# Optimization experiments

Measured on AMD Instinct MI355X. Metric: run time of the kernel, lower is better.

Reference implementation:

```python
import jax, jax.numpy as jnp
import numpy as np

B, C, FH, FW = 8, 256, 64, 64   # sketch/ref feature maps (B, C, F_H, F_W)
N = 131072                       # ~B*FH*FW*4 triplets, as the nested loops produce
MARGIN = 12.0


def setup_inputs() -> dict:
    key = jax.random.key(0)
    k1, k2, k3, k4, k5, k6 = jax.random.split(key, 6)
    sketch_query_vectors = jax.random.normal(k1, (B, C, FH, FW), jnp.float32)
    ref_key_vectors = jax.random.normal(k2, (B, C, FH, FW), jnp.float32)
    # Precomputed triplet indices. In the original these come from GridProcessing
    # (CPU grid math on G + random.choices negatives); they are constants w.r.t.
    # the float inputs, so we sample them once here.
    batch_idx = jax.random.randint(k3, (N,), 0, B, jnp.int32)
    anchor_yx = jax.random.randint(k4, (N, 2), 0, FH, jnp.int32)
    pos_yx = jax.random.randint(k5, (N, 2), 0, FH, jnp.int32)
    neg_yx = jax.random.randint(k6, (N, 2), 0, FH, jnp.int32)
    return {
        "sketch_query_vectors": sketch_query_vectors,
        "ref_key_vectors": ref_key_vectors,
        "batch_idx": batch_idx,
        "anchor_yx": anchor_yx,
        "pos_yx": pos_yx,
        "neg_yx": neg_yx,
    }


def reference(sketch_query_vectors, ref_key_vectors, batch_idx, anchor_yx, pos_yx, neg_yx):
    # Gather per-triplet feature vectors: [N, C]
    a = sketch_query_vectors[batch_idx, :, anchor_yx[:, 0], anchor_yx[:, 1]]
    p = ref_key_vectors[batch_idx, :, pos_yx[:, 0], pos_yx[:, 1]]
    n = ref_key_vectors[batch_idx, :, neg_yx[:, 0], neg_yx[:, 1]]
    dp = jnp.sum((a - p) ** 2, axis=-1)  # squared-euclidean, as calc_euclidean
    dn = jnp.sum((a - n) ** 2, axis=-1)
    losses = jax.nn.relu(dp - dn + MARGIN)  # per-triplet hinge (1-elem mean in orig)
    return jnp.sum(losses) / (1e-6 + N)
```

## Files before the change

kernel.cpp:

```cpp
#include <hip/hip_runtime.h>

#define NB 8
#define NC 256
#define FH 64
#define FW 64
#define NS (FH * FW)
#define NSAMP 131072
#define MARGIN_F 12.0f
#define GATHER_BLOCKS (NSAMP / 32)

typedef float vfloat2 __attribute__((ext_vector_type(2)));

__device__ __forceinline__ unsigned pack4_fp8(float f0, float f1, float f2, float f3)
{
    int r = __builtin_amdgcn_cvt_pk_fp8_f32(f0, f1, 0, false);
    r     = __builtin_amdgcn_cvt_pk_fp8_f32(f2, f3, r, true);
    return (unsigned)r;
}

__global__ __launch_bounds__(256) void transpose_to_bsc_fp8(
    const float* __restrict__ in0, const float* __restrict__ in1,
    unsigned char* __restrict__ out0, unsigned char* __restrict__ out1)
{
    __shared__ float tile[64][65];

    const int which = blockIdx.z >> 3;
    const int b     = blockIdx.z & 7;
    const float* __restrict__ in  = which ? in1 : in0;
    unsigned char* __restrict__ out = which ? out1 : out0;

    const int s0 = blockIdx.x * 64;
    const int c0 = blockIdx.y * 64;
    const int t  = threadIdx.x;

    const float* __restrict__ inb  = in  + (size_t)b * NC * NS;
    unsigned char* __restrict__ outb = out + (size_t)b * NS * NC;

    const int g   = t >> 4;
    const int sl4 = (t & 15) << 2;
#pragma unroll
    for (int pass = 0; pass < 4; ++pass) {
        const int cl = pass * 16 + g;
        const float4 v = *(const float4*)&inb[(size_t)(c0 + cl) * NS + (s0 + sl4)];
        tile[sl4 + 0][cl] = v.x;
        tile[sl4 + 1][cl] = v.y;
        tile[sl4 + 2][cl] = v.z;
        tile[sl4 + 3][cl] = v.w;
    }
    __syncthreads();

    const int cl4 = (t & 15) << 2;
#pragma unroll
    for (int pass = 0; pass < 4; ++pass) {
        const int sl = pass * 16 + (t >> 4);
        const unsigned w = pack4_fp8(tile[sl][cl4 + 0], tile[sl][cl4 + 1],
                                     tile[sl][cl4 + 2], tile[sl][cl4 + 3]);
        *(unsigned*)&outb[(size_t)(s0 + sl) * NC + (c0 + cl4)] = w;
    }
}

__device__ __forceinline__ void acc_u32(unsigned a, unsigned p, unsigned n, float& d)
{
    const vfloat2 a0 = __builtin_amdgcn_cvt_pk_f32_fp8(a, false);
    const vfloat2 a1 = __builtin_amdgcn_cvt_pk_f32_fp8(a, true);
    const vfloat2 p0 = __builtin_amdgcn_cvt_pk_f32_fp8(p, false);
    const vfloat2 p1 = __builtin_amdgcn_cvt_pk_f32_fp8(p, true);
    const vfloat2 n0 = __builtin_amdgcn_cvt_pk_f32_fp8(n, false);
    const vfloat2 n1 = __builtin_amdgcn_cvt_pk_f32_fp8(n, true);
    float t;
    t = a0.x - p0.x; d += t * t;  t = a0.x - n0.x; d -= t * t;
    t = a0.y - p0.y; d += t * t;  t = a0.y - n0.y; d -= t * t;
    t = a1.x - p1.x; d += t * t;  t = a1.x - n1.x; d -= t * t;
    t = a1.y - p1.y; d += t * t;  t = a1.y - n1.y; d -= t * t;
}

__device__ __forceinline__ void acc_quad(uint4 a, uint4 p, uint4 n, float& d)
{
    acc_u32(a.x, p.x, n.x, d);
    acc_u32(a.y, p.y, n.y, d);
    acc_u32(a.z, p.z, n.z, d);
    acc_u32(a.w, p.w, n.w, d);
}

__global__ __launch_bounds__(256) void triplet_gather_fp8(
    const uint4* __restrict__ tq,
    const uint4* __restrict__ tk,
    const int*  __restrict__ batch_idx,
    const int2* __restrict__ anchor_yx,
    const int2* __restrict__ pos_yx,
    const int2* __restrict__ neg_yx,
    float* __restrict__ partials)
{
    const int t    = threadIdx.x;
    const int ol   = t & 7;
    const int oct  = t >> 3;
    const int samp = blockIdx.x * 32 + oct;

    const int  b  = batch_idx[samp];
    const int2 ay = anchor_yx[samp];
    const int2 py = pos_yx[samp];
    const int2 ny = neg_yx[samp];

    const size_t ab = ((size_t)(b * NS) + ay.x * FW + ay.y) * 16;
    const size_t pb = ((size_t)(b * NS) + py.x * FW + py.y) * 16;
    const size_t nb = ((size_t)(b * NS) + ny.x * FW + ny.y) * 16;

    const uint4 A0 = tq[ab + ol];
    const uint4 A1 = tq[ab + 8 + ol];
    const uint4 P0 = tk[pb + ol];
    const uint4 P1 = tk[pb + 8 + ol];
    const uint4 N0 = tk[nb + ol];
    const uint4 N1 = tk[nb + 8 + ol];

    float d = 0.0f;
    acc_quad(A0, P0, N0, d);
    acc_quad(A1, P1, N1, d);

#pragma unroll
    for (int m = 1; m < 8; m <<= 1) d += __shfl_xor(d, m, 64);

    __shared__ float part[32];
    if (ol == 0) part[oct] = fmaxf(d + MARGIN_F, 0.0f);
    __syncthreads();
    if (t == 0) {
        float s = 0.0f;
#pragma unroll
        for (int i = 0; i < 32; ++i) s += part[i];
        partials[blockIdx.x] = s;
    }
}

__global__ __launch_bounds__(256) void final_reduce(
    const float* __restrict__ partials, float* __restrict__ out)
{
    float s = 0.0f;
    for (int i = threadIdx.x; i < GATHER_BLOCKS; i += 256) s += partials[i];
#pragma unroll
    for (int m = 1; m < 64; m <<= 1) s += __shfl_xor(s, m, 64);
    __shared__ float ws4[4];
    if ((threadIdx.x & 63) == 0) ws4[threadIdx.x >> 6] = s;
    __syncthreads();
    if (threadIdx.x == 0) {
        const float invN = 1.0f / (1e-6f + (float)NSAMP);
        out[0] = (ws4[0] + ws4[1] + ws4[2] + ws4[3]) * invN;
    }
}

__global__ __launch_bounds__(256) void triplet_direct(
    const float* __restrict__ q, const float* __restrict__ k,
    const int*  __restrict__ batch_idx,
    const int2* __restrict__ anchor_yx,
    const int2* __restrict__ pos_yx,
    const int2* __restrict__ neg_yx,
    float* __restrict__ out)
{
    const int lane   = threadIdx.x & 63;
    const int wid    = threadIdx.x >> 6;
    const int gwave  = blockIdx.x * 4 + wid;
    const int nwaves = gridDim.x * 4;

    float wsum = 0.0f;
    for (int i = gwave; i < NSAMP; i += nwaves) {
        const int  b  = batch_idx[i];
        const int2 ay = anchor_yx[i];
        const int2 py = pos_yx[i];
        const int2 ny = neg_yx[i];

        const size_t base = (size_t)b * NC * NS;
        const int sa = ay.x * FW + ay.y;
        const int sp = py.x * FW + py.y;
        const int sn = ny.x * FW + ny.y;

        float d = 0.0f;
#pragma unroll
        for (int kk = 0; kk < 4; ++kk) {
            const int c = lane + 64 * kk;
            const float av = q[base + (size_t)c * NS + sa];
            const float pv = k[base + (size_t)c * NS + sp];
            const float nv = k[base + (size_t)c * NS + sn];
            float t;
            t = av - pv; d += t * t;
            t = av - nv; d -= t * t;
        }
#pragma unroll
        for (int m = 1; m < 64; m <<= 1) d += __shfl_xor(d, m, 64);
        if (lane == 0) wsum += fmaxf(d + MARGIN_F, 0.0f);
    }

    __shared__ float bsum[4];
    if (lane == 0) bsum[wid] = wsum;
    __syncthreads();
    if (threadIdx.x == 0) {
        const float invN = 1.0f / (1e-6f + (float)NSAMP);
        atomicAdd(out, (bsum[0] + bsum[1] + bsum[2] + bsum[3]) * invN);
    }
}

extern "C" void kernel_launch(void* const* d_in, const int* in_sizes, int n_in,
                              void* d_out, int out_size, void* d_ws, size_t ws_size,
                              hipStream_t stream)
{
    const float* sketch = (const float*)d_in[0];
    const float* refk   = (const float*)d_in[1];
    const int*   bidx   = (const int*)d_in[2];
    const int2*  ayx    = (const int2*)d_in[3];
    const int2*  pyx    = (const int2*)d_in[4];
    const int2*  nyx    = (const int2*)d_in[5];
    float*       out    = (float*)d_out;

    const size_t tensor_elems = (size_t)NB * NC * NS;
    const size_t need = 2 * tensor_elems * sizeof(unsigned char)
                      + GATHER_BLOCKS * sizeof(float);

    if (ws_size >= need) {
        unsigned char* tq = (unsigned char*)d_ws;
        unsigned char* tk = tq + tensor_elems;
        float* partials = (float*)(tk + tensor_elems);

        dim3 tgrid(NS / 64, NC / 64, 16);
        transpose_to_bsc_fp8<<<tgrid, 256, 0, stream>>>(sketch, refk, tq, tk);

        triplet_gather_fp8<<<GATHER_BLOCKS, 256, 0, stream>>>(
            (const uint4*)tq, (const uint4*)tk, bidx, ayx, pyx, nyx, partials);

        final_reduce<<<1, 256, 0, stream>>>(partials, out);
    } else {
        (void)hipMemsetAsync(out, 0, sizeof(float), stream);
        triplet_direct<<<4096, 256, 0, stream>>>(
            sketch, refk, bidx, ayx, pyx, nyx, out);
    }
}
```

Measured before the change: 123.3 us.

## Bucket triplets by batch so each XCD gathers from one batch slice

Adds a bucketing pass that sorts triplet index records by batch into per-batch arrays using shared and global atomic cursors. The gather kernel then maps blockIdx&7 to a batch, so under round-robin XCD dispatch each XCD only touches one batch's fp8 feature slice, which should improve L2 locality. The final reduce kernel is replaced by an atomicAdd per block. The cost is an extra kernel, two memsets, record writes and reads, and a data-dependent strided loop. The mapping assumes blocks are dispatched to XCDs round-robin.

Measured after the change: 170.1 us. 1.38x slower.

```diff
diff --git a/kernel.cpp b/kernel.cpp
--- a/kernel.cpp
+++ b/kernel.cpp
@@ -7,7 +7,12 @@
 #define NS (FH * FW)
 #define NSAMP 131072
 #define MARGIN_F 12.0f
-#define GATHER_BLOCKS (NSAMP / 32)
+
+#define BUCKET_CAP NSAMP
+#define GATHER_BLOCKS 4096
+#define GROUPS_PER_XCD (GATHER_BLOCKS / 8)
+#define OCTETS_PER_BLOCK 32
+#define BUCKET_STRIDE (GROUPS_PER_XCD * OCTETS_PER_BLOCK)
 
 typedef float vfloat2 __attribute__((ext_vector_type(2)));
 
@@ -57,6 +62,35 @@
                                      tile[sl][cl4 + 2], tile[sl][cl4 + 3]);
         *(unsigned*)&outb[(size_t)(s0 + sl) * NC + (c0 + cl4)] = w;
     }
+}
+
+__global__ __launch_bounds__(256) void bucket_samples(
+    const int*  __restrict__ batch_idx,
+    const int2* __restrict__ anchor_yx,
+    const int2* __restrict__ pos_yx,
+    const int2* __restrict__ neg_yx,
+    uint4* __restrict__ recs,
+    unsigned* __restrict__ cursors)
+{
+    const int i = blockIdx.x * 256 + threadIdx.x;
+    const int  b  = batch_idx[i];
+    const int2 ay = anchor_yx[i];
+    const int2 py = pos_yx[i];
+    const int2 ny = neg_yx[i];
+
+    const unsigned aoff = (unsigned)(b * NS + ay.x * FW + ay.y);
+    const unsigned poff = (unsigned)(b * NS + py.x * FW + py.y);
+    const unsigned noff = (unsigned)(b * NS + ny.x * FW + ny.y);
+
+    __shared__ unsigned hist[8], base[8];
+    if (threadIdx.x < 8) hist[threadIdx.x] = 0;
+    __syncthreads();
+    const unsigned rank = atomicAdd(&hist[b], 1u);
+    __syncthreads();
+    if (threadIdx.x < 8)
+        base[threadIdx.x] = atomicAdd(&cursors[threadIdx.x], hist[threadIdx.x]);
+    __syncthreads();
+    recs[(size_t)b * BUCKET_CAP + base[b] + rank] = make_uint4(aoff, poff, noff, 0u);
 }
 
 __device__ __forceinline__ void acc_u32(unsigned a, unsigned p, unsigned n, float& d)
@@ -82,67 +116,52 @@
     acc_u32(a.w, p.w, n.w, d);
 }
 
-__global__ __launch_bounds__(256) void triplet_gather_fp8(
+__global__ __launch_bounds__(256) void triplet_gather_xcd(
     const uint4* __restrict__ tq,
     const uint4* __restrict__ tk,
-    const int*  __restrict__ batch_idx,
-    const int2* __restrict__ anchor_yx,
-    const int2* __restrict__ pos_yx,
-    const int2* __restrict__ neg_yx,
-    float* __restrict__ partials)
-{
-    const int t    = threadIdx.x;
-    const int ol   = t & 7;
-    const int oct  = t >> 3;
-    const int samp = blockIdx.x * 32 + oct;
-
-    const int  b  = batch_idx[samp];
-    const int2 ay = anchor_yx[samp];
-    const int2 py = pos_yx[samp];
-    const int2 ny = neg_yx[samp];
-
-    const size_t ab = ((size_t)(b * NS) + ay.x * FW + ay.y) * 16;
-    const size_t pb = ((size_t)(b * NS) + py.x * FW + py.y) * 16;
-    const size_t nb = ((size_t)(b * NS) + ny.x * FW + ny.y) * 16;
-
-    const uint4 A0 = tq[ab + ol];
-    const uint4 A1 = tq[ab + 8 + ol];
-    const uint4 P0 = tk[pb + ol];
-    const uint4 P1 = tk[pb + 8 + ol];
-    const uint4 N0 = tk[nb + ol];
-    const uint4 N1 = tk[nb + 8 + ol];
-
-    float d = 0.0f;
-    acc_quad(A0, P0, N0, d);
-    acc_quad(A1, P1, N1, d);
-
-#pragma unroll
-    for (int m = 1; m < 8; m <<= 1) d += __shfl_xor(d, m, 64);
-
-    __shared__ float part[32];
-    if (ol == 0) part[oct] = fmaxf(d + MARGIN_F, 0.0f);
+    const uint4* __restrict__ recs,
+    const unsigned* __restrict__ cursors,
+    float* __restrict__ out)
+{
+    const int t   = threadIdx.x;
+    const int ol  = t & 7;
+    const int oct = t >> 3;
+    const int x   = blockIdx.x & 7;
+    const int g   = blockIdx.x >> 3;
+
+    const unsigned cnt = cursors[x];
+    const uint4* __restrict__ brecs = recs + (size_t)x * BUCKET_CAP;
+
+    float acc = 0.0f;
+    for (unsigned j = (unsigned)(g * OCTETS_PER_BLOCK + oct); j < cnt; j += BUCKET_STRIDE) {
+        const uint4 r = brecs[j];
+        const size_t ab = (size_t)r.x * 16;
+        const size_t pb = (size_t)r.y * 16;
+        const size_t nb = (size_t)r.z * 16;
+
+        const uint4 A0 = tq[ab + ol];
+        const uint4 A1 = tq[ab + 8 + ol];
+        const uint4 P0 = tk[pb + ol];
+        const uint4 P1 = tk[pb + 8 + ol];
+        const uint4 N0 = tk[nb + ol];
+        const uint4 N1 = tk[nb + 8 + ol];
+
+        float d = 0.0f;
+        acc_quad(A0, P0, N0, d);
+        acc_quad(A1, P1, N1, d);
+#pragma unroll
+        for (int m = 1; m < 8; m <<= 1) d += __shfl_xor(d, m, 64);
+        acc += (ol == 0) ? fmaxf(d + MARGIN_F, 0.0f) : 0.0f;
+    }
+
+#pragma unroll
+    for (int m = 1; m < 64; m <<= 1) acc += __shfl_xor(acc, m, 64);
+    __shared__ float wsum[4];
+    if ((t & 63) == 0) wsum[t >> 6] = acc;
     __syncthreads();
     if (t == 0) {
-        float s = 0.0f;
-#pragma unroll
-        for (int i = 0; i < 32; ++i) s += part[i];
-        partials[blockIdx.x] = s;
-    }
-}
-
-__global__ __launch_bounds__(256) void final_reduce(
-    const float* __restrict__ partials, float* __restrict__ out)
-{
-    float s = 0.0f;
-    for (int i = threadIdx.x; i < GATHER_BLOCKS; i += 256) s += partials[i];
-#pragma unroll
-    for (int m = 1; m < 64; m <<= 1) s += __shfl_xor(s, m, 64);
-    __shared__ float ws4[4];
-    if ((threadIdx.x & 63) == 0) ws4[threadIdx.x >> 6] = s;
-    __syncthreads();
-    if (threadIdx.x == 0) {
         const float invN = 1.0f / (1e-6f + (float)NSAMP);
-        out[0] = (ws4[0] + ws4[1] + ws4[2] + ws4[3]) * invN;
+        atomicAdd(out, (wsum[0] + wsum[1] + wsum[2] + wsum[3]) * invN);
     }
 }
 
@@ -208,24 +227,29 @@
     const int2*  nyx    = (const int2*)d_in[5];
     float*       out    = (float*)d_out;
 
+    (void)hipMemsetAsync(out, 0, sizeof(float), stream);
+
     const size_t tensor_elems = (size_t)NB * NC * NS;
-    const size_t need = 2 * tensor_elems * sizeof(unsigned char)
-                      + GATHER_BLOCKS * sizeof(float);
+    const size_t recs_bytes   = (size_t)NB * BUCKET_CAP * sizeof(uint4);
+    const size_t need = 2 * tensor_elems + recs_bytes + 8 * sizeof(unsigned);
 
     if (ws_size >= need) {
         unsigned char* tq = (unsigned char*)d_ws;
         unsigned char* tk = tq + tensor_elems;
-        float* partials = (float*)(tk + tensor_elems);
+        uint4* recs       = (uint4*)(tk + tensor_elems);
+        unsigned* cursors = (unsigned*)((unsigned char*)recs + recs_bytes);
+
+        (void)hipMemsetAsync(cursors, 0, 8 * sizeof(unsigned), stream);
 
         dim3 tgrid(NS / 64, NC / 64, 16);
         transpose_to_bsc_fp8<<<tgrid, 256, 0, stream>>>(sketch, refk, tq, tk);
 
-        triplet_gather_fp8<<<GATHER_BLOCKS, 256, 0, stream>>>(
-            (const uint4*)tq, (const uint4*)tk, bidx, ayx, pyx, nyx, partials);
-
-        final_reduce<<<1, 256, 0, stream>>>(partials, out);
+        bucket_samples<<<NSAMP / 256, 256, 0, stream>>>(
+            bidx, ayx, pyx, nyx, recs, cursors);
+
+        triplet_gather_xcd<<<GATHER_BLOCKS, 256, 0, stream>>>(
+            (const uint4*)tq, (const uint4*)tk, recs, cursors, out);
     } else {
-        (void)hipMemsetAsync(out, 0, sizeof(float), stream);
         triplet_direct<<<4096, 256, 0, stream>>>(
             sketch, refk, bidx, ayx, pyx, nyx, out);
     }
```

## Fuse transpose, gather and reduction into one cooperative persistent kernel

Applied to the files above, without the earlier changes.

Merges the fp8 transpose, the triplet gather and the final reduction into a single cooperative kernel. A persistent grid loops over the transpose tiles, waits at a grid-wide sync, then runs a grid-strided loop over the triplets. The final sum is built with a packed 64-bit atomic that holds a fixed-point sum plus a block counter, and the last block to arrive writes the mean. This removes two kernel launches and the partials buffer, but it adds grid-sync overhead, relies on fixed-point rounding of each block's partial, and assumes the hard-coded 256 compute units when it sizes the grid.

New measurement: 211.0 us. +71.1%, slower.

```diff
diff --git a/kernel.cpp b/kernel.cpp
--- a/kernel.cpp
+++ b/kernel.cpp
@@ -1,4 +1,7 @@
 #include <hip/hip_runtime.h>
+#include <hip/hip_cooperative_groups.h>
+
+namespace cg = cooperative_groups;
 
 #define NB 8
 #define NC 256
@@ -7,7 +10,7 @@
 #define NS (FH * FW)
 #define NSAMP 131072
 #define MARGIN_F 12.0f
-#define GATHER_BLOCKS (NSAMP / 32)
+#define NTILES 4096
 
 typedef float vfloat2 __attribute__((ext_vector_type(2)));
 
@@ -16,47 +19,6 @@
     int r = __builtin_amdgcn_cvt_pk_fp8_f32(f0, f1, 0, false);
     r     = __builtin_amdgcn_cvt_pk_fp8_f32(f2, f3, r, true);
     return (unsigned)r;
-}
-
-__global__ __launch_bounds__(256) void transpose_to_bsc_fp8(
-    const float* __restrict__ in0, const float* __restrict__ in1,
-    unsigned char* __restrict__ out0, unsigned char* __restrict__ out1)
-{
-    __shared__ float tile[64][65];
-
-    const int which = blockIdx.z >> 3;
-    const int b     = blockIdx.z & 7;
-    const float* __restrict__ in  = which ? in1 : in0;
-    unsigned char* __restrict__ out = which ? out1 : out0;
-
-    const int s0 = blockIdx.x * 64;
-    const int c0 = blockIdx.y * 64;
-    const int t  = threadIdx.x;
-
-    const float* __restrict__ inb  = in  + (size_t)b * NC * NS;
-    unsigned char* __restrict__ outb = out + (size_t)b * NS * NC;
-
-    const int g   = t >> 4;
-    const int sl4 = (t & 15) << 2;
-#pragma unroll
-    for (int pass = 0; pass < 4; ++pass) {
-        const int cl = pass * 16 + g;
-        const float4 v = *(const float4*)&inb[(size_t)(c0 + cl) * NS + (s0 + sl4)];
-        tile[sl4 + 0][cl] = v.x;
-        tile[sl4 + 1][cl] = v.y;
-        tile[sl4 + 2][cl] = v.z;
-        tile[sl4 + 3][cl] = v.w;
-    }
-    __syncthreads();
-
-    const int cl4 = (t & 15) << 2;
-#pragma unroll
-    for (int pass = 0; pass < 4; ++pass) {
-        const int sl = pass * 16 + (t >> 4);
-        const unsigned w = pack4_fp8(tile[sl][cl4 + 0], tile[sl][cl4 + 1],
-                                     tile[sl][cl4 + 2], tile[sl][cl4 + 3]);
-        *(unsigned*)&outb[(size_t)(s0 + sl) * NC + (c0 + cl4)] = w;
-    }
 }
 
 __device__ __forceinline__ void acc_u32(unsigned a, unsigned p, unsigned n, float& d)
@@ -82,67 +44,108 @@
     acc_u32(a.w, p.w, n.w, d);
 }
 
-__global__ __launch_bounds__(256) void triplet_gather_fp8(
-    const uint4* __restrict__ tq,
-    const uint4* __restrict__ tk,
+__global__ __launch_bounds__(256) void triplet_fused(
+    const float* __restrict__ in0, const float* __restrict__ in1,
+    unsigned char* __restrict__ tq8, unsigned char* __restrict__ tk8,
     const int*  __restrict__ batch_idx,
     const int2* __restrict__ anchor_yx,
     const int2* __restrict__ pos_yx,
     const int2* __restrict__ neg_yx,
-    float* __restrict__ partials)
-{
-    const int t    = threadIdx.x;
-    const int ol   = t & 7;
-    const int oct  = t >> 3;
-    const int samp = blockIdx.x * 32 + oct;
-
-    const int  b  = batch_idx[samp];
-    const int2 ay = anchor_yx[samp];
-    const int2 py = pos_yx[samp];
-    const int2 ny = neg_yx[samp];
-
-    const size_t ab = ((size_t)(b * NS) + ay.x * FW + ay.y) * 16;
-    const size_t pb = ((size_t)(b * NS) + py.x * FW + py.y) * 16;
-    const size_t nb = ((size_t)(b * NS) + ny.x * FW + ny.y) * 16;
-
-    const uint4 A0 = tq[ab + ol];
-    const uint4 A1 = tq[ab + 8 + ol];
-    const uint4 P0 = tk[pb + ol];
-    const uint4 P1 = tk[pb + 8 + ol];
-    const uint4 N0 = tk[nb + ol];
-    const uint4 N1 = tk[nb + 8 + ol];
-
-    float d = 0.0f;
-    acc_quad(A0, P0, N0, d);
-    acc_quad(A1, P1, N1, d);
-
-#pragma unroll
-    for (int m = 1; m < 8; m <<= 1) d += __shfl_xor(d, m, 64);
-
-    __shared__ float part[32];
-    if (ol == 0) part[oct] = fmaxf(d + MARGIN_F, 0.0f);
+    unsigned long long* __restrict__ ctrl,
+    float* __restrict__ out)
+{
+    __shared__ float tile[64][65];
+    const int t = threadIdx.x;
+
+    if (blockIdx.x == 0 && t == 0) atomicExch(ctrl, 0ull);
+
+    for (int tl = blockIdx.x; tl < NTILES; tl += gridDim.x) {
+        __syncthreads();
+        const int xt    = tl & 63;
+        const int yt    = (tl >> 6) & 3;
+        const int zt    = tl >> 8;
+        const int which = zt >> 3;
+        const int b     = zt & 7;
+        const float* __restrict__ in  = which ? in1 : in0;
+        unsigned char* __restrict__ o = which ? tk8 : tq8;
+
+        const int s0 = xt * 64;
+        const int c0 = yt * 64;
+        const float* __restrict__ inb  = in + (size_t)b * NC * NS;
+        unsigned char* __restrict__ outb = o + (size_t)b * NS * NC;
+
+        const int g   = t >> 4;
+        const int sl4 = (t & 15) << 2;
+#pragma unroll
+        for (int pass = 0; pass < 4; ++pass) {
+            const int cl = pass * 16 + g;
+            const float4 v = *(const float4*)&inb[(size_t)(c0 + cl) * NS + (s0 + sl4)];
+            tile[sl4 + 0][cl] = v.x;
+            tile[sl4 + 1][cl] = v.y;
+            tile[sl4 + 2][cl] = v.z;
+            tile[sl4 + 3][cl] = v.w;
+        }
+        __syncthreads();
+
+        const int cl4 = (t & 15) << 2;
+#pragma unroll
+        for (int pass = 0; pass < 4; ++pass) {
+            const int sl = pass * 16 + (t >> 4);
+            const unsigned w = pack4_fp8(tile[sl][cl4 + 0], tile[sl][cl4 + 1],
+                                         tile[sl][cl4 + 2], tile[sl][cl4 + 3]);
+            *(unsigned*)&outb[(size_t)(s0 + sl) * NC + (c0 + cl4)] = w;
+        }
+    }
+
+    cg::this_grid().sync();
+
+    const uint4* __restrict__ tq = (const uint4*)tq8;
+    const uint4* __restrict__ tk = (const uint4*)tk8;
+    const int ol  = t & 7;
+    const int oct = t >> 3;
+
+    float acc = 0.0f;
+    for (int s = blockIdx.x * 32 + oct; s < NSAMP; s += gridDim.x * 32) {
+        const int  b  = batch_idx[s];
+        const int2 ay = anchor_yx[s];
+        const int2 py = pos_yx[s];
+        const int2 ny = neg_yx[s];
+
+        const size_t ab = ((size_t)(b * NS) + ay.x * FW + ay.y) * 16;
+        const size_t pb = ((size_t)(b * NS) + py.x * FW + py.y) * 16;
+        const size_t nb = ((size_t)(b * NS) + ny.x * FW + ny.y) * 16;
+
+        const uint4 A0 = tq[ab + ol];
+        const uint4 A1 = tq[ab + 8 + ol];
+        const uint4 P0 = tk[pb + ol];
+        const uint4 P1 = tk[pb + 8 + ol];
+        const uint4 N0 = tk[nb + ol];
+        const uint4 N1 = tk[nb + 8 + ol];
+
+        float d = 0.0f;
+        acc_quad(A0, P0, N0, d);
+        acc_quad(A1, P1, N1, d);
+#pragma unroll
+        for (int m = 1; m < 8; m <<= 1) d += __shfl_xor(d, m, 64);
+        if (ol == 0) acc += fmaxf(d + MARGIN_F, 0.0f);
+    }
+
+#pragma unroll
+    for (int m = 1; m < 64; m <<= 1) acc += __shfl_xor(acc, m, 64);
+    __shared__ float wsum[4];
+    if ((t & 63) == 0) wsum[t >> 6] = acc;
     __syncthreads();
+
     if (t == 0) {
-        float s = 0.0f;
-#pragma unroll
-        for (int i = 0; i < 32; ++i) s += part[i];
-        partials[blockIdx.x] = s;
-    }
-}
-
-__global__ __launch_bounds__(256) void final_reduce(
-    const float* __restrict__ partials, float* __restrict__ out)
-{
-    float s = 0.0f;
-    for (int i = threadIdx.x; i < GATHER_BLOCKS; i += 256) s += partials[i];
-#pragma unroll
-    for (int m = 1; m < 64; m <<= 1) s += __shfl_xor(s, m, 64);
-    __shared__ float ws4[4];
-    if ((threadIdx.x & 63) == 0) ws4[threadIdx.x >> 6] = s;
-    __syncthreads();
-    if (threadIdx.x == 0) {
-        const float invN = 1.0f / (1e-6f + (float)NSAMP);
-        out[0] = (ws4[0] + ws4[1] + ws4[2] + ws4[3]) * invN;
+        const float part = wsum[0] + wsum[1] + wsum[2] + wsum[3];
+        const unsigned long long fx =
+            (unsigned long long)(part * 1048576.0f + 0.5f);
+        const unsigned long long packed = (1ull << 52) | fx;
+        const unsigned long long newv = atomicAdd(ctrl, packed) + packed;
+        if ((unsigned)(newv >> 52) == gridDim.x) {
+            const double sum = (double)(newv & ((1ull << 52) - 1)) * (1.0 / 1048576.0);
+            out[0] = (float)(sum / (1e-6 + (double)NSAMP));
+        }
     }
 }
 
@@ -209,21 +212,27 @@
     float*       out    = (float*)d_out;
 
     const size_t tensor_elems = (size_t)NB * NC * NS;
-    const size_t need = 2 * tensor_elems * sizeof(unsigned char)
-                      + GATHER_BLOCKS * sizeof(float);
+    const size_t need = 2 * tensor_elems + sizeof(unsigned long long);
 
     if (ws_size >= need) {
         unsigned char* tq = (unsigned char*)d_ws;
         unsigned char* tk = tq + tensor_elems;
-        float* partials = (float*)(tk + tensor_elems);
-
-        dim3 tgrid(NS / 64, NC / 64, 16);
-        transpose_to_bsc_fp8<<<tgrid, 256, 0, stream>>>(sketch, refk, tq, tk);
-
-        triplet_gather_fp8<<<GATHER_BLOCKS, 256, 0, stream>>>(
-            (const uint4*)tq, (const uint4*)tk, bidx, ayx, pyx, nyx, partials);
-
-        final_reduce<<<1, 256, 0, stream>>>(partials, out);
+        unsigned long long* ctrl = (unsigned long long*)(tk + tensor_elems);
+
+        int maxb = 0;
+        if (hipOccupancyMaxActiveBlocksPerMultiprocessor(
+                &maxb, (const void*)triplet_fused, 256, 0) != hipSuccess || maxb < 1)
+            maxb = 4;
+        int G = maxb * 256;
+        if (G > 2048) G = 2048;
+
+        void* args[] = {
+            (void*)&sketch, (void*)&refk, (void*)&tq, (void*)&tk,
+            (void*)&bidx, (void*)&ayx, (void*)&pyx, (void*)&nyx,
+            (void*)&ctrl, (void*)&out
+        };
+        (void)hipLaunchCooperativeKernel((const void*)triplet_fused,
+                                         dim3(G), dim3(256), args, 0, stream);
     } else {
         (void)hipMemsetAsync(out, 0, sizeof(float), stream);
         triplet_direct<<<4096, 256, 0, stream>>>(
```
